# Kernel optimization log

Hardware: AMD Instinct MI355X
Metric: run time of the kernel (lower is better)

The kernel has to match this reference:

```python
import jax, jax.numpy as jnp
import numpy as np

NITER = 20
TOL = 1e-10


def setup_inputs() -> dict:
    key = jax.random.key(0)
    n = 8192
    kA, kR, kX = jax.random.split(key, 3)
    # SPD, well-conditioned system matrix: M = A A^T / n + I
    A = jax.random.normal(kA, (n, n), dtype=jnp.float32) * np.float32(1.0 / np.sqrt(n))
    M = A @ A.T + jnp.eye(n, dtype=jnp.float32)
    RHS = jax.random.normal(kR, (n,), dtype=jnp.float32)
    X = jax.random.normal(kX, (n,), dtype=jnp.float32)  # only its shape is used (zeros_like)
    return {"X": X, "M": M, "RHS": RHS}


def reference(X, M, RHS):
    # Faithful port of the TF while_loop CG: max NITER iterations,
    # early-stop condition rTr > 1e-10 emulated by freezing the state
    # (where-select) once converged, keeping fixed shapes under jit.
    X0 = jnp.zeros_like(X)
    r0 = RHS - M @ X0
    p0 = r0
    rTr0 = jnp.sum(r0 * r0)

    def body(carry, _):
        rTr, Xc, r, p = carry
        Ap = M @ p                      # [n] matvec, dominant cost
        rtr = jnp.sum(r * r)            # recomputed in loop body, as in TF source
        alpha = rtr / jnp.sum(p * Ap)
        Xn = Xc + alpha * p
        rn = r - alpha * Ap
        beta = jnp.sum(rn * rn) / rtr
        pn = rn + beta * p
        rTrn = jnp.sum(rn * rn)
        active = rTr > TOL              # while_loop cond on rTr from previous iter
        sel = lambda new, old: jnp.where(active, new, old)
        return (sel(rTrn, rTr), sel(Xn, Xc), sel(rn, r), sel(pn, p)), None

    (_, Xf, _, _), _ = jax.lax.scan(body, (rTr0, X0, r0, p0), None, length=NITER)
    return Xf
```

## Files before the change

kernel.cpp:

```cpp
#include <hip/hip_runtime.h>

#define N 8192
#define NITER 20
#define TOLF 1e-10f

typedef float floatx4 __attribute__((ext_vector_type(4)));
typedef unsigned int uintx4 __attribute__((ext_vector_type(4)));

__device__ __forceinline__ unsigned short f2bf_rne(float f) {
  unsigned int u = __float_as_uint(f);
  unsigned int r = u + 0x7fffu + ((u >> 16) & 1u);
  return (unsigned short)(r >> 16);
}
__device__ __forceinline__ unsigned int pk_bf2(float lo, float hi) {
  return (unsigned int)f2bf_rne(lo) | ((unsigned int)f2bf_rne(hi) << 16);
}
__device__ __forceinline__ float bflo(unsigned int u) { return __uint_as_float(u << 16); }
__device__ __forceinline__ float bfhi(unsigned int u) { return __uint_as_float(u & 0xffff0000u); }

__device__ __forceinline__ float lds_pget(const float* pAf, const float* pBf, int c) {
  int idx = ((c >> 3) << 2) | (c & 3);
  return (c & 4) ? pBf[idx] : pAf[idx];
}

__global__ __launch_bounds__(256) void init_kernel(
    const float* __restrict__ RHS, float* __restrict__ x, float* __restrict__ r,
    float* __restrict__ rt0) {
  int i = blockIdx.x * 256 + threadIdx.x;
  float v = RHS[i];
  x[i] = 0.0f;
  r[i] = v;
  float val = v * v;
  for (int off = 32; off > 0; off >>= 1) val += __shfl_down(val, off, 64);
  __shared__ float bs[4];
  int wave = threadIdx.x >> 6, lane = threadIdx.x & 63;
  if (lane == 0) bs[wave] = val;
  __syncthreads();
  if (threadIdx.x == 0) atomicAdd(rt0, bs[0] + bs[1] + bs[2] + bs[3]);
}

__device__ __forceinline__ void matvec_tail(
    float acc0, float acc1, int row0,
    const float* pAf, const float* pBf,
    float* __restrict__ Ap, float* pap, float* bsP) {
  int wave = threadIdx.x >> 6, lane = threadIdx.x & 63;
  for (int off = 32; off > 0; off >>= 1) {
    acc0 += __shfl_down(acc0, off, 64);
    acc1 += __shfl_down(acc1, off, 64);
  }
  if (lane == 0) {
    Ap[row0]     = acc0;
    Ap[row0 + 1] = acc1;
    bsP[wave] = lds_pget(pAf, pBf, row0) * acc0
              + lds_pget(pAf, pBf, row0 + 1) * acc1;
  }
  __syncthreads();
  if (threadIdx.x == 0) {
    float SP = 0.f;
#pragma unroll
    for (int w = 0; w < 16; ++w) SP += bsP[w];
    atomicAdd(pap, SP);
  }
}

__global__ __launch_bounds__(1024, 4) void matvec0_cast(
    const float* __restrict__ M, unsigned short* __restrict__ Mb,
    const float* __restrict__ RHS, float* __restrict__ p0,
    float* __restrict__ Ap, float* __restrict__ pap) {
  __shared__ floatx4 pA[1024], pB[1024];
  __shared__ float bsP[16];
  int b = blockIdx.x, t = threadIdx.x;
  int c = t * 8;
  floatx4 va = *(const floatx4*)(RHS + c);
  floatx4 vb = *(const floatx4*)(RHS + c + 4);
  pA[t] = va;
  pB[t] = vb;
  if ((t >> 2) == b) {
    *(floatx4*)(p0 + c) = va;
    *(floatx4*)(p0 + c + 4) = vb;
  }
  __syncthreads();

  int wave = t >> 6, lane = t & 63;
  int row0 = b * 32 + wave * 2;
  const float* M0 = M + (size_t)row0 * N;
  const float* M1 = M0 + N;
  unsigned short* B0 = Mb + (size_t)row0 * N;
  unsigned short* B1 = B0 + N;
  float acc0 = 0.f, acc1 = 0.f;
#pragma unroll 2
  for (int s = 0; s < 16; ++s) {
    int cc = s * 512 + lane * 8;
    floatx4 a0 = *(const floatx4*)(M0 + cc);
    floatx4 a1 = *(const floatx4*)(M0 + cc + 4);
    floatx4 b0 = *(const floatx4*)(M1 + cc);
    floatx4 b1 = *(const floatx4*)(M1 + cc + 4);
    floatx4 pa = pA[s * 64 + lane];
    floatx4 pb = pB[s * 64 + lane];
    acc0 += a0.x*pa.x + a0.y*pa.y + a0.z*pa.z + a0.w*pa.w
          + a1.x*pb.x + a1.y*pb.y + a1.z*pb.z + a1.w*pb.w;
    acc1 += b0.x*pa.x + b0.y*pa.y + b0.z*pa.z + b0.w*pa.w
          + b1.x*pb.x + b1.y*pb.y + b1.z*pb.z + b1.w*pb.w;
    uintx4 o0 = {pk_bf2(a0.x, a0.y), pk_bf2(a0.z, a0.w),
                 pk_bf2(a1.x, a1.y), pk_bf2(a1.z, a1.w)};
    uintx4 o1 = {pk_bf2(b0.x, b0.y), pk_bf2(b0.z, b0.w),
                 pk_bf2(b1.x, b1.y), pk_bf2(b1.z, b1.w)};
    *(uintx4*)(B0 + cc) = o0;
    *(uintx4*)(B1 + cc) = o1;
  }
  matvec_tail(acc0, acc1, row0, (const float*)pA, (const float*)pB, Ap, pap, bsP);
}

__global__ __launch_bounds__(1024, 4) void matvec_step(
    const unsigned short* __restrict__ Mb, const float* __restrict__ r,
    const float* __restrict__ p_old, float* __restrict__ p_new,
    float* __restrict__ Ap, const float* __restrict__ rt_prev,
    const float* __restrict__ rt_cur, float* __restrict__ pap) {
  __shared__ floatx4 pA[1024], pB[1024];
  __shared__ float bsP[16];
  int b = blockIdx.x, t = threadIdx.x;
  int c = t * 8;

  float rtc = *rt_cur;
  if (!(rtc > TOLF)) {
    if ((t >> 2) == b) {
      *(floatx4*)(p_new + c)     = *(const floatx4*)(p_old + c);
      *(floatx4*)(p_new + c + 4) = *(const floatx4*)(p_old + c + 4);
    }
    return;
  }
  float beta = rtc / *rt_prev;

  floatx4 rv0 = *(const floatx4*)(r + c);
  floatx4 rv1 = *(const floatx4*)(r + c + 4);
  floatx4 po0 = *(const floatx4*)(p_old + c);
  floatx4 po1 = *(const floatx4*)(p_old + c + 4);
  floatx4 pv0 = rv0 + beta * po0;
  floatx4 pv1 = rv1 + beta * po1;
  pA[t] = pv0;
  pB[t] = pv1;
  if ((t >> 2) == b) {
    *(floatx4*)(p_new + c)     = pv0;
    *(floatx4*)(p_new + c + 4) = pv1;
  }
  __syncthreads();

  int wave = t >> 6, lane = t & 63;
  int row0 = b * 32 + wave * 2;
  const unsigned short* M0 = Mb + (size_t)row0 * N;
  const unsigned short* M1 = M0 + N;
  float acc0 = 0.f, acc1 = 0.f;
#pragma unroll 4
  for (int s = 0; s < 16; ++s) {
    int cc = s * 512 + lane * 8;
    uintx4 m0 = *(const uintx4*)(M0 + cc);
    uintx4 m1 = *(const uintx4*)(M1 + cc);
    floatx4 pa = pA[s * 64 + lane];
    floatx4 pb = pB[s * 64 + lane];
    acc0 += bflo(m0.x) * pa.x + bfhi(m0.x) * pa.y
          + bflo(m0.y) * pa.z + bfhi(m0.y) * pa.w
          + bflo(m0.z) * pb.x + bfhi(m0.z) * pb.y
          + bflo(m0.w) * pb.z + bfhi(m0.w) * pb.w;
    acc1 += bflo(m1.x) * pa.x + bfhi(m1.x) * pa.y
          + bflo(m1.y) * pa.z + bfhi(m1.y) * pa.w
          + bflo(m1.z) * pb.x + bfhi(m1.z) * pb.y
          + bflo(m1.w) * pb.z + bfhi(m1.w) * pb.w;
  }
  matvec_tail(acc0, acc1, row0, (const float*)pA, (const float*)pB, Ap, pap, bsP);
}

__global__ __launch_bounds__(256) void update_ew(
    const float* __restrict__ Ap, const float* __restrict__ p,
    float* __restrict__ x, float* __restrict__ r,
    const float* __restrict__ rt, const float* __restrict__ pap,
    float* __restrict__ rt_next) {
  float rtv = *rt;
  bool act = rtv > TOLF;
  if (!act) {
    if (blockIdx.x == 0 && threadIdx.x == 0) *rt_next = rtv;
    return;
  }
  float a = rtv / *pap;
  int base = (blockIdx.x * 256 + threadIdx.x) * 4;
  floatx4 pv = *(const floatx4*)(p + base);
  floatx4 av = *(const floatx4*)(Ap + base);
  floatx4 xv = *(const floatx4*)(x + base);
  floatx4 rv = *(const floatx4*)(r + base);
  xv += a * pv;
  rv -= a * av;
  *(floatx4*)(x + base) = xv;
  *(floatx4*)(r + base) = rv;
  float val = rv.x * rv.x + rv.y * rv.y + rv.z * rv.z + rv.w * rv.w;
  for (int off = 32; off > 0; off >>= 1) val += __shfl_down(val, off, 64);
  __shared__ float bs[4];
  int wave = threadIdx.x >> 6, lane = threadIdx.x & 63;
  if (lane == 0) bs[wave] = val;
  __syncthreads();
  if (threadIdx.x == 0) atomicAdd(rt_next, bs[0] + bs[1] + bs[2] + bs[3]);
}

extern "C" void kernel_launch(void* const* d_in, const int* in_sizes, int n_in,
                              void* d_out, int out_size, void* d_ws, size_t ws_size,
                              hipStream_t stream) {
  const float* M   = (const float*)d_in[1];
  const float* RHS = (const float*)d_in[2];
  float* x = (float*)d_out;

  char* ws = (char*)d_ws;
  unsigned short* Mb = (unsigned short*)ws;
  float* Ap = (float*)(ws + (size_t)N * N * 2);
  float* r  = Ap + N;
  float* P0 = r + N;
  float* P1 = P0 + N;
  float* sc = P1 + N;
  float* RT  = sc;
  float* PAP = sc + 21;

  (void)hipMemsetAsync(sc, 0, 41 * sizeof(float), stream);

  float* P[2] = {P0, P1};

  init_kernel<<<N / 256, 256, 0, stream>>>(RHS, x, r, &RT[0]);
  matvec0_cast<<<N / 32, 1024, 0, stream>>>(M, Mb, RHS, P[0], Ap, &PAP[0]);
  update_ew<<<N / 1024, 256, 0, stream>>>(Ap, P[0], x, r, &RT[0], &PAP[0], &RT[1]);
  for (int k = 1; k < NITER; ++k) {
    matvec_step<<<N / 32, 1024, 0, stream>>>(Mb, r, P[(k - 1) & 1], P[k & 1],
                                             Ap, &RT[k - 1], &RT[k], &PAP[k]);
    update_ew<<<N / 1024, 256, 0, stream>>>(Ap, P[k & 1], x, r, &RT[k],
                                            &PAP[k], &RT[k + 1]);
  }
}
```

Baseline: 876.7 us.

## Fuse CG vector update and residual reduction into each matvec kernel

Removes the separate elementwise update kernel and init kernel by having every matvec block redundantly recompute the residual update r -= alpha*Ap and its full norm over all N elements before forming p. Each block then writes only its own slice of x, r and p, and a small final kernel applies the last x update. This roughly halves the number of kernel launches and removes the atomic-based rTr reduction. The cost is redundant reading of r, p and Ap (about 96KB) per block and an extra block-wide reduction on the critical path before the matvec.

```diff
diff --git a/kernel.cpp b/kernel.cpp
--- a/kernel.cpp
+++ b/kernel.cpp
@@ -23,20 +23,15 @@
   return (c & 4) ? pBf[idx] : pAf[idx];
 }
 
-__global__ __launch_bounds__(256) void init_kernel(
-    const float* __restrict__ RHS, float* __restrict__ x, float* __restrict__ r,
-    float* __restrict__ rt0) {
-  int i = blockIdx.x * 256 + threadIdx.x;
-  float v = RHS[i];
-  x[i] = 0.0f;
-  r[i] = v;
-  float val = v * v;
+__device__ __forceinline__ float block_sum_1024(float val, float* red) {
   for (int off = 32; off > 0; off >>= 1) val += __shfl_down(val, off, 64);
-  __shared__ float bs[4];
   int wave = threadIdx.x >> 6, lane = threadIdx.x & 63;
-  if (lane == 0) bs[wave] = val;
+  if (lane == 0) red[wave] = val;
   __syncthreads();
-  if (threadIdx.x == 0) atomicAdd(rt0, bs[0] + bs[1] + bs[2] + bs[3]);
+  float S = 0.f;
+#pragma unroll
+  for (int w = 0; w < 16; ++w) S += red[w];
+  return S;
 }
 
 __device__ __forceinline__ void matvec_tail(
@@ -63,12 +58,12 @@
   }
 }
 
-__global__ __launch_bounds__(1024, 4) void matvec0_cast(
+__global__ __launch_bounds__(1024, 4) void cg_first(
     const float* __restrict__ M, unsigned short* __restrict__ Mb,
-    const float* __restrict__ RHS, float* __restrict__ p0,
-    float* __restrict__ Ap, float* __restrict__ pap) {
+    const float* __restrict__ RHS, float* __restrict__ x,
+    float* __restrict__ ap0, float* __restrict__ rt0, float* __restrict__ pap0) {
   __shared__ floatx4 pA[1024], pB[1024];
-  __shared__ float bsP[16];
+  __shared__ float redA[16], bsP[16];
   int b = blockIdx.x, t = threadIdx.x;
   int c = t * 8;
   floatx4 va = *(const floatx4*)(RHS + c);
@@ -76,10 +71,14 @@
   pA[t] = va;
   pB[t] = vb;
   if ((t >> 2) == b) {
-    *(floatx4*)(p0 + c) = va;
-    *(floatx4*)(p0 + c + 4) = vb;
-  }
-  __syncthreads();
+    floatx4 z = {0.f, 0.f, 0.f, 0.f};
+    *(floatx4*)(x + c) = z;
+    *(floatx4*)(x + c + 4) = z;
+  }
+  float val = va.x*va.x + va.y*va.y + va.z*va.z + va.w*va.w
+            + vb.x*vb.x + vb.y*vb.y + vb.z*vb.z + vb.w*vb.w;
+  float rt = block_sum_1024(val, redA);
+  if (b == 0 && t == 0) *rt0 = rt;
 
   int wave = t >> 6, lane = t & 63;
   int row0 = b * 32 + wave * 2;
@@ -108,42 +107,66 @@
     *(uintx4*)(B0 + cc) = o0;
     *(uintx4*)(B1 + cc) = o1;
   }
-  matvec_tail(acc0, acc1, row0, (const float*)pA, (const float*)pB, Ap, pap, bsP);
-}
-
-__global__ __launch_bounds__(1024, 4) void matvec_step(
-    const unsigned short* __restrict__ Mb, const float* __restrict__ r,
+  matvec_tail(acc0, acc1, row0, (const float*)pA, (const float*)pB, ap0, pap0, bsP);
+}
+
+__global__ __launch_bounds__(1024, 4) void cg_fused(
+    const unsigned short* __restrict__ Mb,
+    const float* __restrict__ r_old, float* __restrict__ r_new,
     const float* __restrict__ p_old, float* __restrict__ p_new,
-    float* __restrict__ Ap, const float* __restrict__ rt_prev,
-    const float* __restrict__ rt_cur, float* __restrict__ pap) {
+    const float* __restrict__ ap_old, float* __restrict__ ap_new,
+    float* __restrict__ x,
+    const float* __restrict__ rt_prev_p, const float* __restrict__ pap_prev_p,
+    float* __restrict__ rt_out, float* __restrict__ pap_out) {
   __shared__ floatx4 pA[1024], pB[1024];
-  __shared__ float bsP[16];
+  __shared__ float redA[16], bsP[16];
   int b = blockIdx.x, t = threadIdx.x;
   int c = t * 8;
 
-  float rtc = *rt_cur;
-  if (!(rtc > TOLF)) {
-    if ((t >> 2) == b) {
-      *(floatx4*)(p_new + c)     = *(const floatx4*)(p_old + c);
-      *(floatx4*)(p_new + c + 4) = *(const floatx4*)(p_old + c + 4);
-    }
-    return;
-  }
-  float beta = rtc / *rt_prev;
-
-  floatx4 rv0 = *(const floatx4*)(r + c);
-  floatx4 rv1 = *(const floatx4*)(r + c + 4);
+  float rt_prev = *rt_prev_p;
+  bool act_prev = rt_prev > TOLF;
+  float alpha = act_prev ? rt_prev / *pap_prev_p : 0.0f;
+
+  floatx4 ro0 = *(const floatx4*)(r_old + c);
+  floatx4 ro1 = *(const floatx4*)(r_old + c + 4);
   floatx4 po0 = *(const floatx4*)(p_old + c);
   floatx4 po1 = *(const floatx4*)(p_old + c + 4);
-  floatx4 pv0 = rv0 + beta * po0;
-  floatx4 pv1 = rv1 + beta * po1;
+  floatx4 ao0 = *(const floatx4*)(ap_old + c);
+  floatx4 ao1 = *(const floatx4*)(ap_old + c + 4);
+
+  floatx4 rv0 = act_prev ? (ro0 - alpha * ao0) : ro0;
+  floatx4 rv1 = act_prev ? (ro1 - alpha * ao1) : ro1;
+
+  float val = rv0.x*rv0.x + rv0.y*rv0.y + rv0.z*rv0.z + rv0.w*rv0.w
+            + rv1.x*rv1.x + rv1.y*rv1.y + rv1.z*rv1.z + rv1.w*rv1.w;
+  float rn = block_sum_1024(val, redA);
+  float rn_rep = act_prev ? rn : rt_prev;
+  bool act = rn_rep > TOLF;
+  float beta = act_prev ? rn / rt_prev : 0.0f;
+
+  floatx4 pv0 = act_prev ? (rv0 + beta * po0) : po0;
+  floatx4 pv1 = act_prev ? (rv1 + beta * po1) : po1;
   pA[t] = pv0;
   pB[t] = pv1;
+
   if ((t >> 2) == b) {
+    if (act_prev) {
+      floatx4 xv0 = *(const floatx4*)(x + c);
+      floatx4 xv1 = *(const floatx4*)(x + c + 4);
+      xv0 += alpha * po0;
+      xv1 += alpha * po1;
+      *(floatx4*)(x + c) = xv0;
+      *(floatx4*)(x + c + 4) = xv1;
+    }
+    *(floatx4*)(r_new + c)     = rv0;
+    *(floatx4*)(r_new + c + 4) = rv1;
     *(floatx4*)(p_new + c)     = pv0;
     *(floatx4*)(p_new + c + 4) = pv1;
   }
+  if (b == 0 && t == 0) *rt_out = rn_rep;
   __syncthreads();
+
+  if (!act) return;
 
   int wave = t >> 6, lane = t & 63;
   int row0 = b * 32 + wave * 2;
@@ -166,37 +189,21 @@
           + bflo(m1.z) * pb.x + bfhi(m1.z) * pb.y
           + bflo(m1.w) * pb.z + bfhi(m1.w) * pb.w;
   }
-  matvec_tail(acc0, acc1, row0, (const float*)pA, (const float*)pB, Ap, pap, bsP);
-}
-
-__global__ __launch_bounds__(256) void update_ew(
-    const float* __restrict__ Ap, const float* __restrict__ p,
-    float* __restrict__ x, float* __restrict__ r,
-    const float* __restrict__ rt, const float* __restrict__ pap,
-    float* __restrict__ rt_next) {
-  float rtv = *rt;
-  bool act = rtv > TOLF;
-  if (!act) {
-    if (blockIdx.x == 0 && threadIdx.x == 0) *rt_next = rtv;
-    return;
-  }
-  float a = rtv / *pap;
+  matvec_tail(acc0, acc1, row0, (const float*)pA, (const float*)pB,
+              ap_new, pap_out, bsP);
+}
+
+__global__ __launch_bounds__(256) void cg_final(
+    float* __restrict__ x, const float* __restrict__ p_last,
+    const float* __restrict__ rt_ptr, const float* __restrict__ pap_ptr) {
+  float rt = *rt_ptr;
+  if (!(rt > TOLF)) return;
+  float a = rt / *pap_ptr;
   int base = (blockIdx.x * 256 + threadIdx.x) * 4;
-  floatx4 pv = *(const floatx4*)(p + base);
-  floatx4 av = *(const floatx4*)(Ap + base);
   floatx4 xv = *(const floatx4*)(x + base);
-  floatx4 rv = *(const floatx4*)(r + base);
+  floatx4 pv = *(const floatx4*)(p_last + base);
   xv += a * pv;
-  rv -= a * av;
   *(floatx4*)(x + base) = xv;
-  *(floatx4*)(r + base) = rv;
-  float val = rv.x * rv.x + rv.y * rv.y + rv.z * rv.z + rv.w * rv.w;
-  for (int off = 32; off > 0; off >>= 1) val += __shfl_down(val, off, 64);
-  __shared__ float bs[4];
-  int wave = threadIdx.x >> 6, lane = threadIdx.x & 63;
-  if (lane == 0) bs[wave] = val;
-  __syncthreads();
-  if (threadIdx.x == 0) atomicAdd(rt_next, bs[0] + bs[1] + bs[2] + bs[3]);
 }
 
 extern "C" void kernel_launch(void* const* d_in, const int* in_sizes, int n_in,
@@ -208,25 +215,31 @@
 
   char* ws = (char*)d_ws;
   unsigned short* Mb = (unsigned short*)ws;
-  float* Ap = (float*)(ws + (size_t)N * N * 2);
-  float* r  = Ap + N;
-  float* P0 = r + N;
+  float* A0 = (float*)(ws + (size_t)N * N * 2);
+  float* A1 = A0 + N;
+  float* R0 = A1 + N;
+  float* R1 = R0 + N;
+  float* P0 = R1 + N;
   float* P1 = P0 + N;
   float* sc = P1 + N;
   float* RT  = sc;
-  float* PAP = sc + 21;
-
-  (void)hipMemsetAsync(sc, 0, 41 * sizeof(float), stream);
-
-  float* P[2] = {P0, P1};
-
-  init_kernel<<<N / 256, 256, 0, stream>>>(RHS, x, r, &RT[0]);
-  matvec0_cast<<<N / 32, 1024, 0, stream>>>(M, Mb, RHS, P[0], Ap, &PAP[0]);
-  update_ew<<<N / 1024, 256, 0, stream>>>(Ap, P[0], x, r, &RT[0], &PAP[0], &RT[1]);
+  float* PAP = sc + 20;
+
+  (void)hipMemsetAsync(sc, 0, 40 * sizeof(float), stream);
+
+  float* Ab[2] = {A0, A1};
+  float* Rb[2] = {R0, R1};
+  float* Pb[2] = {P0, P1};
+
+  cg_first<<<N / 32, 1024, 0, stream>>>(M, Mb, RHS, x, Ab[0], &RT[0], &PAP[0]);
   for (int k = 1; k < NITER; ++k) {
-    matvec_step<<<N / 32, 1024, 0, stream>>>(Mb, r, P[(k - 1) & 1], P[k & 1],
-                                             Ap, &RT[k - 1], &RT[k], &PAP[k]);
-    update_ew<<<N / 1024, 256, 0, stream>>>(Ap, P[k & 1], x, r, &RT[k],
-                                            &PAP[k], &RT[k + 1]);
-  }
-}
+    const float* rold = (k == 1) ? RHS : Rb[(k - 1) & 1];
+    const float* pold = (k == 1) ? RHS : Pb[(k - 1) & 1];
+    cg_fused<<<N / 32, 1024, 0, stream>>>(Mb, rold, Rb[k & 1], pold, Pb[k & 1],
+                                          Ab[(k - 1) & 1], Ab[k & 1], x,
+                                          &RT[k - 1], &PAP[k - 1],
+                                          &RT[k], &PAP[k]);
+  }
+  cg_final<<<N / 1024, 256, 0, stream>>>(x, Pb[(NITER - 1) & 1],
+                                         &RT[NITER - 1], &PAP[NITER - 1]);
+}
```

Result: no change. 864.5 us (-1.4%).
